# Performance work log

Measured on AMD Instinct MI355X. Metric: run time of the kernel, lower is better.

## Reference

```python
import jax, jax.numpy as jnp
import numpy as np
import math

D, H, FF = 1024, 16, 4096
B, L = 4, 1024

def setup_inputs() -> dict:
    key = jax.random.key(0)
    ks = jax.random.split(key, 20)
    g = lambda k, shp: jax.random.normal(k, shp, dtype=jnp.float32) * 0.02
    inp = {
        'x': jax.random.normal(ks[0], (B, L, D), dtype=jnp.float32),
        'encoder_output': jax.random.normal(ks[1], (B, L, D), dtype=jnp.float32),
        'src_mask': jnp.ones((1, 1, L, L), dtype=jnp.int32),
        'tgt_mask': jnp.tril(jnp.ones((L, L), dtype=jnp.int32))[None, None],
        'wq': g(ks[2], (D, D)), 'bq': jnp.zeros((D,), jnp.float32),
        'wk': g(ks[3], (D, D)), 'bk': jnp.zeros((D,), jnp.float32),
        'wv': g(ks[4], (D, D)), 'bv': jnp.zeros((D,), jnp.float32),
        'wo': g(ks[5], (D, D)), 'bo': jnp.zeros((D,), jnp.float32),
        'w1': g(ks[6], (FF, D)), 'b1': jnp.zeros((FF,), jnp.float32),
        'w2': g(ks[7], (D, FF)), 'b2': jnp.zeros((D,), jnp.float32),
        'g1': jnp.ones((D,), jnp.float32), 'be1': jnp.zeros((D,), jnp.float32),
        'g2': jnp.ones((D,), jnp.float32), 'be2': jnp.zeros((D,), jnp.float32),
    }
    return inp

def _layernorm(x, g, b, eps=1e-5):
    mu = jnp.mean(x, axis=-1, keepdims=True)
    var = jnp.var(x, axis=-1, keepdims=True)
    return (x - mu) * jax.lax.rsqrt(var + eps) * g + b

def _mha(q, k, v, mask, wq, bq, wk, bk, wv, bv, wo, bo):
    Bq, Lq, C = q.shape
    dh = C // H
    qh = (q @ wq.T + bq).reshape(Bq, Lq, H, dh)      # b q h d
    kh = (k @ wk.T + bk).reshape(Bq, -1, H, dh)       # b k h d
    vh = (v @ wv.T + bv).reshape(Bq, -1, H, dh)
    # NOTE: source scales by sqrt(C) (full model dim), not sqrt(head_dim)
    scores = jnp.einsum('bqhd,bkhd->bhqk', qh, kh) / math.sqrt(C)
    if mask is not None:
        scores = jnp.where(mask == 0, jnp.float32(-1e9), scores)
    attn = jax.nn.softmax(scores, axis=-1)
    out = jnp.einsum('bhqk,bkhd->bqhd', attn, vh).reshape(Bq, Lq, C)
    return out @ wo.T + bo

def reference(x, encoder_output, src_mask, tgt_mask,
              wq, bq, wk, bk, wv, bv, wo, bo,
              w1, b1, w2, b2, g1, be1, g2, be2):
    # self-attention (dropout identity in eval mode)
    y1 = _mha(x, x, x, tgt_mask, wq, bq, wk, bk, wv, bv, wo, bo)
    y1 = _layernorm(y1 + x, g1, be1)
    # cross-attention: source reuses attn1 weights and layer_norm1 (faithful)
    y2 = _mha(y1, encoder_output, encoder_output, src_mask, wq, bq, wk, bk, wv, bv, wo, bo)
    y2 = _layernorm(y1 + y2, g1, be1)
    # FFN + layer_norm2
    y = jax.nn.relu(y2 @ w1.T + b1) @ w2.T + b2
    return _layernorm(y2 + y, g2, be2)
```

## Files before the change

### kernel.cpp

```cpp
#include <hip/hip_runtime.h>
#include <hip/hip_bf16.h>

typedef __attribute__((ext_vector_type(8))) short short8;
typedef __attribute__((ext_vector_type(4))) float f32x4;
typedef __attribute__((ext_vector_type(4))) unsigned short ushort4v;

#define MFMA_BF16(a, b, c) __builtin_amdgcn_mfma_f32_16x16x32_bf16((a), (b), (c), 0, 0, 0)
#define AS1 __attribute__((address_space(1)))
#define AS3 __attribute__((address_space(3)))

__device__ __forceinline__ unsigned short f2b(float f) {
  unsigned u = __float_as_uint(f);
  u += 0x7fffu + ((u >> 16) & 1u);
  return (unsigned short)(u >> 16);
}

__device__ __forceinline__ size_t kpack_idx(int row, int col) {
  int b = row >> 10, l = row & 1023, h = col >> 6, d = col & 63;
  return ((size_t)(b * 16 + h) << 16) + l * 64 + (d ^ ((l & 7) << 3));
}

__global__ __launch_bounds__(256) void cast8(
    const float* s0, const float* s1, const float* s2, const float* s3,
    const float* s4, const float* s5, const float* s6, const float* s7,
    unsigned short* d0, unsigned short* d1, unsigned short* d2, unsigned short* d3,
    unsigned short* d4, unsigned short* d5, unsigned short* d6, unsigned short* d7,
    int n0, int n1, int n2, int n3, int n4, int n5, int n6, int n7) {
  const float* s; unsigned short* d; int n;
  switch (blockIdx.y) {
    case 0: s = s0; d = d0; n = n0; break;
    case 1: s = s1; d = d1; n = n1; break;
    case 2: s = s2; d = d2; n = n2; break;
    case 3: s = s3; d = d3; n = n3; break;
    case 4: s = s4; d = d4; n = n4; break;
    case 5: s = s5; d = d5; n = n5; break;
    case 6: s = s6; d = d6; n = n6; break;
    default: s = s7; d = d7; n = n7; break;
  }
  int stride = gridDim.x * blockDim.x;
  for (int i = blockIdx.x * blockDim.x + threadIdx.x; i < n; i += stride) {
    float4 v = reinterpret_cast<const float4*>(s)[i];
    ushort4v o;
    o.x = f2b(v.x); o.y = f2b(v.y); o.z = f2b(v.z); o.w = f2b(v.w);
    reinterpret_cast<ushort4v*>(d)[i] = o;
  }
}

template <int RELU, int RES, int OUTF, int OUTB, int TM>
__global__ __launch_bounds__(256) void gemm_bt(
    const unsigned short* __restrict__ A, const unsigned short* __restrict__ W,
    const float* __restrict__ bias, const float* __restrict__ resid,
    float* __restrict__ outF, unsigned short* __restrict__ outB,
    int M, int N, int K) {
  constexpr int MI = TM / 32;
  __shared__ unsigned short lA[TM * 64];
  __shared__ unsigned short lB[128 * 64];
  int nbn = N >> 7;
  int nwg = gridDim.x;
  int id = blockIdx.x;
  { int q = nwg >> 3; id = (id & 7) * q + (id >> 3); }
  int m0 = (id / nbn) * TM, n0 = (id % nbn) << 7;
  int lane = threadIdx.x & 63, wave = threadIdx.x >> 6;
  int wr = (wave >> 1) * (TM / 2), wc = (wave & 1) * 64;
  int rq = lane & 15, kq = (lane >> 4) * 8;
  int xr8 = (rq & 7) << 3;
  f32x4 acc[MI][4] = {};

  int t8 = threadIdx.x * 8;
  for (int kt = 0; kt < K; kt += 64) {
#pragma unroll
    for (int i = 0; i < MI; ++i) {
      int e = t8 + i * 2048;
      int row = e >> 6;
      int gcol = (((e >> 3) & 7) ^ (row & 7)) << 3;
      __builtin_amdgcn_global_load_lds(
          (const AS1 void*)(A + (size_t)(m0 + row) * K + kt + gcol),
          (AS3 void*)(lA + e), 16, 0, 0);
    }
#pragma unroll
    for (int i = 0; i < 4; ++i) {
      int e = t8 + i * 2048;
      int row = e >> 6;
      int gcol = (((e >> 3) & 7) ^ (row & 7)) << 3;
      __builtin_amdgcn_global_load_lds(
          (const AS1 void*)(W + (size_t)(n0 + row) * K + kt + gcol),
          (AS3 void*)(lB + e), 16, 0, 0);
    }
    __syncthreads();
#pragma unroll
    for (int s = 0; s < 2; ++s) {
      short8 af[MI], bf[4];
#pragma unroll
      for (int i = 0; i < MI; ++i)
        af[i] = *reinterpret_cast<const short8*>(lA + (wr + i * 16 + rq) * 64 + ((s * 32 + kq) ^ xr8));
#pragma unroll
      for (int j = 0; j < 4; ++j)
        bf[j] = *reinterpret_cast<const short8*>(lB + (wc + j * 16 + rq) * 64 + ((s * 32 + kq) ^ xr8));
#pragma unroll
      for (int i = 0; i < MI; ++i)
#pragma unroll
        for (int j = 0; j < 4; ++j)
          acc[i][j] = MFMA_BF16(af[i], bf[j], acc[i][j]);
    }
    __syncthreads();
  }

  int r0 = (lane >> 4) * 4;
#pragma unroll
  for (int i = 0; i < MI; ++i) {
#pragma unroll
    for (int j = 0; j < 4; ++j) {
      int row = m0 + wr + i * 16 + r0;
      int col = n0 + wc + j * 16 + rq;
      float bv = bias[col];
#pragma unroll
      for (int r = 0; r < 4; ++r) {
        float v = acc[i][j][r] + bv;
        if (RES) v += resid[(size_t)(row + r) * N + col];
        if (RELU) v = fmaxf(v, 0.0f);
        if (OUTF) outF[(size_t)(row + r) * N + col] = v;
        if (OUTB) outB[(size_t)(row + r) * N + col] = f2b(v);
      }
    }
  }
}

__global__ __launch_bounds__(256) void gemm_qkv(
    const unsigned short* __restrict__ xb, const unsigned short* __restrict__ encb,
    const unsigned short* __restrict__ wq, const unsigned short* __restrict__ wk,
    const unsigned short* __restrict__ wv,
    const float* __restrict__ bq, const float* __restrict__ bk, const float* __restrict__ bv,
    unsigned short* __restrict__ qb, unsigned short* __restrict__ kp1,
    unsigned short* __restrict__ vp1, unsigned short* __restrict__ kp2,
    unsigned short* __restrict__ vp2) {
  __shared__ unsigned short lA[128 * 64];
  __shared__ unsigned short lB[128 * 64];
  int id = blockIdx.x;
  id = (id & 7) * 160 + (id >> 3);
  int im = id / 40, jn = id % 40;
  int sel = jn >> 3;
  int m0 = im << 7, col0 = (jn & 7) << 7;
  const unsigned short* A = (sel < 3) ? xb : encb;
  const unsigned short* Wm = (sel == 0) ? wq : ((sel == 1 || sel == 3) ? wk : wv);
  const float* bias = (sel == 0) ? bq : ((sel == 1 || sel == 3) ? bk : bv);
  int lane = threadIdx.x & 63, wave = threadIdx.x >> 6;
  int wr = (wave >> 1) * 64, wc = (wave & 1) * 64;
  int rq = lane & 15, kq = (lane >> 4) * 8;
  int xr8 = (rq & 7) << 3;
  f32x4 acc[4][4] = {};

  int t8 = threadIdx.x * 8;
  for (int kt = 0; kt < 1024; kt += 64) {
#pragma unroll
    for (int i = 0; i < 4; ++i) {
      int e = t8 + i * 2048;
      int row = e >> 6;
      int gcol = (((e >> 3) & 7) ^ (row & 7)) << 3;
      __builtin_amdgcn_global_load_lds(
          (const AS1 void*)(A + (size_t)(m0 + row) * 1024 + kt + gcol),
          (AS3 void*)(lA + e), 16, 0, 0);
      __builtin_amdgcn_global_load_lds(
          (const AS1 void*)(Wm + (size_t)(col0 + row) * 1024 + kt + gcol),
          (AS3 void*)(lB + e), 16, 0, 0);
    }
    __syncthreads();
#pragma unroll
    for (int s = 0; s < 2; ++s) {
      short8 af[4], bf[4];
#pragma unroll
      for (int i = 0; i < 4; ++i)
        af[i] = *reinterpret_cast<const short8*>(lA + (wr + i * 16 + rq) * 64 + ((s * 32 + kq) ^ xr8));
#pragma unroll
      for (int j = 0; j < 4; ++j)
        bf[j] = *reinterpret_cast<const short8*>(lB + (wc + j * 16 + rq) * 64 + ((s * 32 + kq) ^ xr8));
#pragma unroll
      for (int i = 0; i < 4; ++i)
#pragma unroll
        for (int j = 0; j < 4; ++j)
          acc[i][j] = MFMA_BF16(af[i], bf[j], acc[i][j]);
    }
    __syncthreads();
  }

  unsigned short* outp = (sel == 0) ? qb : (sel == 1) ? kp1 : (sel == 2) ? vp1
                         : (sel == 3) ? kp2 : vp2;
  int pack = (sel == 0) ? 0 : ((sel == 1 || sel == 3) ? 1 : 2);
  int r0 = (lane >> 4) * 4;
#pragma unroll
  for (int i = 0; i < 4; ++i) {
#pragma unroll
    for (int j = 0; j < 4; ++j) {
      int row0 = m0 + wr + i * 16 + r0;
      int col = col0 + wc + j * 16 + rq;
      float bv = bias[col];
      if (pack == 2) {
        int b = row0 >> 10, k0 = row0 & 1023, h = col >> 6, d = col & 63;
        size_t idx = ((size_t)((b * 16 + h) * 16 + (k0 >> 6)) << 12) + d * 64 + ((k0 & 63) ^ ((d & 7) << 3));
        ushort4v o;
        o.x = f2b(acc[i][j][0] + bv);
        o.y = f2b(acc[i][j][1] + bv);
        o.z = f2b(acc[i][j][2] + bv);
        o.w = f2b(acc[i][j][3] + bv);
        *reinterpret_cast<ushort4v*>(&outp[idx]) = o;
      } else {
#pragma unroll
        for (int r = 0; r < 4; ++r) {
          int row = row0 + r;
          float v = acc[i][j][r] + bv;
          if (pack == 0) outp[(size_t)row * 1024 + col] = f2b(v);
          else outp[kpack_idx(row, col)] = f2b(v);
        }
      }
    }
  }
}

__device__ __forceinline__ void attn_step(
    const unsigned short* __restrict__ kcur, const unsigned short* __restrict__ vcur,
    unsigned short* __restrict__ plw, const short8* qf,
    f32x4* accd, float& m2, float& lsum,
    int rq, int hi, int kq, int xr, int wave, bool domask) {
  const float SC = 0.04508422f;
  f32x4 st[4];
#pragma unroll
  for (int sub = 0; sub < 4; ++sub) {
    f32x4 z = {0.f, 0.f, 0.f, 0.f};
#pragma unroll
    for (int c = 0; c < 2; ++c) {
      short8 kf = *reinterpret_cast<const short8*>(
          &kcur[(sub * 16 + rq) * 64 + ((c * 32 + hi * 8) ^ xr)]);
      z = MFMA_BF16(kf, qf[c], z);
    }
    st[sub] = z * SC;
  }
  if (domask) {
#pragma unroll
    for (int sub = 0; sub < 4; ++sub)
#pragma unroll
      for (int r = 0; r < 4; ++r)
        if (sub * 16 + hi * 4 + r > wave * 16 + rq) st[sub][r] = -1e9f;
  }
  f32x4 t0 = {fmaxf(st[0][0], st[1][0]), fmaxf(st[0][1], st[1][1]),
              fmaxf(st[0][2], st[1][2]), fmaxf(st[0][3], st[1][3])};
  f32x4 t1 = {fmaxf(st[2][0], st[3][0]), fmaxf(st[2][1], st[3][1]),
              fmaxf(st[2][2], st[3][2]), fmaxf(st[2][3], st[3][3])};
  float mx = fmaxf(fmaxf(fmaxf(t0[0], t1[0]), fmaxf(t0[1], t1[1])),
                   fmaxf(fmaxf(t0[2], t1[2]), fmaxf(t0[3], t1[3])));
  mx = fmaxf(mx, __shfl_xor(mx, 16, 64));
  mx = fmaxf(mx, __shfl_xor(mx, 32, 64));
  float mn = fmaxf(m2, mx);
  float al = exp2f(m2 - mn);
  m2 = mn;
  f32x4 e[4];
#pragma unroll
  for (int sub = 0; sub < 4; ++sub)
#pragma unroll
    for (int r = 0; r < 4; ++r) e[sub][r] = exp2f(st[sub][r] - mn);
  f32x4 s01 = e[0] + e[1], s23 = e[2] + e[3];
  f32x4 s = s01 + s23;
  float ps = (s[0] + s[1]) + (s[2] + s[3]);
  ps += __shfl_xor(ps, 16, 64);
  ps += __shfl_xor(ps, 32, 64);
  lsum = lsum * al + ps;
#pragma unroll
  for (int sub = 0; sub < 4; ++sub) {
    unsigned w0 = (unsigned)f2b(e[sub][0]) | ((unsigned)f2b(e[sub][1]) << 16);
    unsigned w1 = (unsigned)f2b(e[sub][2]) | ((unsigned)f2b(e[sub][3]) << 16);
    uint2 w = make_uint2(w0, w1);
    *reinterpret_cast<uint2*>(&plw[rq * 64 + ((sub * 16 + hi * 4) ^ xr)]) = w;
  }
  float alb[4];
#pragma unroll
  for (int r = 0; r < 4; ++r) alb[r] = __shfl(al, hi * 4 + r, 64);
#pragma unroll
  for (int d = 0; d < 4; ++d)
#pragma unroll
    for (int r = 0; r < 4; ++r) accd[d][r] *= alb[r];
  short8 pf[2];
#pragma unroll
  for (int c = 0; c < 2; ++c)
    pf[c] = *reinterpret_cast<const short8*>(&plw[rq * 64 + ((c * 32 + hi * 8) ^ xr)]);
#pragma unroll
  for (int d = 0; d < 4; ++d) {
#pragma unroll
    for (int c = 0; c < 2; ++c) {
      short8 vf = *reinterpret_cast<const short8*>(
          &vcur[(d * 16 + rq) * 64 + ((c * 32 + hi * 8) ^ xr)]);
      accd[d] = MFMA_BF16(pf[c], vf, accd[d]);
    }
  }
}

__global__ __launch_bounds__(256) void attn_kernel(
    const unsigned short* __restrict__ Q, const unsigned short* __restrict__ Kp,
    const unsigned short* __restrict__ Vp, unsigned short* __restrict__ O, int causal) {
  __shared__ unsigned short kls[2][4096];
  __shared__ unsigned short vls[2][4096];
  __shared__ unsigned short pls[4][1024];
  int id = blockIdx.x;
  int xcd = id & 7, j = id >> 3;
  int bh = xcd * 8 + (j & 7);
  int b = bh >> 4, h = bh & 15;
  int lane = threadIdx.x & 63, wave = threadIdx.x >> 6;
  int rq = lane & 15, hi = lane >> 4, kq = hi * 8;
  int xr = (rq & 7) << 3;
  int sb = wave * 1024 + lane * 8;
  const unsigned short* Kbh = Kp + ((size_t)bh << 16);
  const unsigned short* Vbh = Vp + ((size_t)bh << 16);
  unsigned short* plw = pls[wave];

  int p = j >> 3;
  int qtA = p;
  int qtB = causal ? (15 - p) : (p + 8);
  int lastA = causal ? qtA : 15;
  int nkt = causal ? (qtB + 1) : 16;

  int qrowA = qtA * 64 + wave * 16, qrowB = qtB * 64 + wave * 16;
  short8 qfA[2], qfB[2];
#pragma unroll
  for (int c = 0; c < 2; ++c) {
    qfA[c] = *reinterpret_cast<const short8*>(
        Q + (size_t)(b * 1024 + qrowA + rq) * 1024 + h * 64 + c * 32 + kq);
    qfB[c] = *reinterpret_cast<const short8*>(
        Q + (size_t)(b * 1024 + qrowB + rq) * 1024 + h * 64 + c * 32 + kq);
  }

  float mA = -1e30f, lsA = 0.f, mB = -1e30f, lsB = 0.f;
  f32x4 accA[4] = {}, accB[4] = {};

#pragma unroll
  for (int i = 0; i < 2; ++i) {
    __builtin_amdgcn_global_load_lds((const AS1 void*)(Kbh + sb + i * 512),
                                     (AS3 void*)(&kls[0][sb + i * 512]), 16, 0, 0);
    __builtin_amdgcn_global_load_lds((const AS1 void*)(Vbh + sb + i * 512),
                                     (AS3 void*)(&vls[0][sb + i * 512]), 16, 0, 0);
  }
  __syncthreads();

  int cur = 0;
  for (int kt = 0; kt < nkt; ++kt) {
    if (kt + 1 < nkt) {
      const unsigned short* kg = Kbh + (kt + 1) * 4096 + sb;
      const unsigned short* vg = Vbh + (kt + 1) * 4096 + sb;
#pragma unroll
      for (int i = 0; i < 2; ++i) {
        __builtin_amdgcn_global_load_lds((const AS1 void*)(kg + i * 512),
                                         (AS3 void*)(&kls[cur ^ 1][sb + i * 512]), 16, 0, 0);
        __builtin_amdgcn_global_load_lds((const AS1 void*)(vg + i * 512),
                                         (AS3 void*)(&vls[cur ^ 1][sb + i * 512]), 16, 0, 0);
      }
    }
    attn_step(kls[cur], vls[cur], plw, qfB, accB, mB, lsB, rq, hi, kq, xr, wave,
              causal && kt == qtB);
    if (kt <= lastA)
      attn_step(kls[cur], vls[cur], plw, qfA, accA, mA, lsA, rq, hi, kq, xr, wave,
                causal && kt == qtA);
    __syncthreads();
    cur ^= 1;
  }

  float lbA[4], lbB[4];
#pragma unroll
  for (int r = 0; r < 4; ++r) {
    lbA[r] = 1.0f / __shfl(lsA, hi * 4 + r, 64);
    lbB[r] = 1.0f / __shfl(lsB, hi * 4 + r, 64);
  }
#pragma unroll
  for (int d = 0; d < 4; ++d)
#pragma unroll
    for (int r = 0; r < 4; ++r) {
      O[(size_t)(b * 1024 + qrowA + hi * 4 + r) * 1024 + h * 64 + d * 16 + rq] =
          f2b(accA[d][r] * lbA[r]);
      O[(size_t)(b * 1024 + qrowB + hi * 4 + r) * 1024 + h * 64 + d * 16 + rq] =
          f2b(accB[d][r] * lbB[r]);
    }
}

template <int OUTF, int OUTB>
__global__ __launch_bounds__(256) void ln_kernel(const float* __restrict__ X,
                                                 const float* __restrict__ g,
                                                 const float* __restrict__ be,
                                                 float* __restrict__ outF,
                                                 unsigned short* __restrict__ outB) {
  __shared__ float red[2][4];
  int row = blockIdx.x;
  int t = threadIdx.x;
  const float* xr = X + (size_t)row * 1024;
  float4 v = reinterpret_cast<const float4*>(xr)[t];
  float s = v.x + v.y + v.z + v.w;
  float ss = v.x * v.x + v.y * v.y + v.z * v.z + v.w * v.w;
#pragma unroll
  for (int off = 1; off < 64; off <<= 1) {
    s += __shfl_xor(s, off, 64);
    ss += __shfl_xor(ss, off, 64);
  }
  int wave = t >> 6;
  if ((t & 63) == 0) { red[0][wave] = s; red[1][wave] = ss; }
  __syncthreads();
  s = red[0][0] + red[0][1] + red[0][2] + red[0][3];
  ss = red[1][0] + red[1][1] + red[1][2] + red[1][3];
  float mu = s * (1.f / 1024.f);
  float var = ss * (1.f / 1024.f) - mu * mu;
  float rs = rsqrtf(var + 1e-5f);
  float4 gv = reinterpret_cast<const float4*>(g)[t];
  float4 bv = reinterpret_cast<const float4*>(be)[t];
  float o0 = (v.x - mu) * rs * gv.x + bv.x;
  float o1 = (v.y - mu) * rs * gv.y + bv.y;
  float o2 = (v.z - mu) * rs * gv.z + bv.z;
  float o3 = (v.w - mu) * rs * gv.w + bv.w;
  if (OUTF) {
    float4 o = make_float4(o0, o1, o2, o3);
    reinterpret_cast<float4*>(outF + (size_t)row * 1024)[t] = o;
  }
  if (OUTB) {
    ushort4v o;
    o.x = f2b(o0); o.y = f2b(o1); o.z = f2b(o2); o.w = f2b(o3);
    reinterpret_cast<ushort4v*>(outB + (size_t)row * 1024)[t] = o;
  }
}

extern "C" void kernel_launch(void* const* d_in, const int* in_sizes, int n_in,
                              void* d_out, int out_size, void* d_ws, size_t ws_size,
                              hipStream_t stream) {
  const float* x   = (const float*)d_in[0];
  const float* enc = (const float*)d_in[1];
  const float* wq = (const float*)d_in[4];  const float* bq = (const float*)d_in[5];
  const float* wk = (const float*)d_in[6];  const float* bk = (const float*)d_in[7];
  const float* wv = (const float*)d_in[8];  const float* bv = (const float*)d_in[9];
  const float* wo = (const float*)d_in[10]; const float* bo = (const float*)d_in[11];
  const float* w1 = (const float*)d_in[12]; const float* b1 = (const float*)d_in[13];
  const float* w2 = (const float*)d_in[14]; const float* b2 = (const float*)d_in[15];
  const float* g1 = (const float*)d_in[16]; const float* be1 = (const float*)d_in[17];
  const float* g2 = (const float*)d_in[18]; const float* be2 = (const float*)d_in[19];
  float* out = (float*)d_out;

  const int M = 4096;
  char* ws = (char*)d_ws;
  size_t off = 0;
  auto alloc = [&](size_t bytes) -> char* {
    char* p = ws + off;
    off += (bytes + 255) & ~(size_t)255;
    return p;
  };
  unsigned short* xb   = (unsigned short*)alloc((size_t)M * 1024 * 2);
  unsigned short* encb = (unsigned short*)alloc((size_t)M * 1024 * 2);
  unsigned short* wqb  = (unsigned short*)alloc((size_t)1024 * 1024 * 2);
  unsigned short* wkb  = (unsigned short*)alloc((size_t)1024 * 1024 * 2);
  unsigned short* wvb  = (unsigned short*)alloc((size_t)1024 * 1024 * 2);
  unsigned short* wob  = (unsigned short*)alloc((size_t)1024 * 1024 * 2);
  unsigned short* w1b  = (unsigned short*)alloc((size_t)4096 * 1024 * 2);
  unsigned short* w2b  = (unsigned short*)alloc((size_t)4096 * 1024 * 2);
  unsigned short* qb   = (unsigned short*)alloc((size_t)M * 1024 * 2);
  unsigned short* kp1  = (unsigned short*)alloc((size_t)M * 1024 * 2);
  unsigned short* vp1  = (unsigned short*)alloc((size_t)M * 1024 * 2);
  unsigned short* kp2  = (unsigned short*)alloc((size_t)M * 1024 * 2);
  unsigned short* vp2  = (unsigned short*)alloc((size_t)M * 1024 * 2);
  unsigned short* ab   = (unsigned short*)alloc((size_t)M * 1024 * 2);
  float* s1 = (float*)alloc((size_t)M * 1024 * 4);
  float* y1 = (float*)alloc((size_t)M * 1024 * 4);
  unsigned short* hb = kp1;
  unsigned short* y1b = xb;
  unsigned short* y2b = qb;
  float* y2 = y1;

  dim3 b256(256);
  cast8<<<dim3(256, 8), b256, 0, stream>>>(
      x, enc, wq, wk, wv, wo, w1, w2,
      xb, encb, wqb, wkb, wvb, wob, w1b, w2b,
      M * 1024 / 4, M * 1024 / 4, 262144, 262144, 262144, 262144,
      4096 * 1024 / 4, 4096 * 1024 / 4);

  gemm_qkv<<<1280, b256, 0, stream>>>(xb, encb, wqb, wkb, wvb, bq, bk, bv,
                                      qb, kp1, vp1, kp2, vp2);

  attn_kernel<<<512, b256, 0, stream>>>(qb, kp1, vp1, ab, 1);
  gemm_bt<0, 1, 1, 0, 64><<<512, b256, 0, stream>>>(ab, wob, bo, x, s1, nullptr, M, 1024, 1024);
  ln_kernel<1, 1><<<4096, b256, 0, stream>>>(s1, g1, be1, y1, y1b);

  gemm_bt<0, 0, 0, 1, 64><<<512, b256, 0, stream>>>(y1b, wqb, bq, nullptr, nullptr, qb, M, 1024, 1024);
  attn_kernel<<<512, b256, 0, stream>>>(qb, kp2, vp2, ab, 0);
  gemm_bt<0, 1, 1, 0, 64><<<512, b256, 0, stream>>>(ab, wob, bo, y1, s1, nullptr, M, 1024, 1024);
  ln_kernel<1, 1><<<4096, b256, 0, stream>>>(s1, g1, be1, y2, y2b);

  gemm_bt<1, 0, 0, 1, 128><<<1024, b256, 0, stream>>>(y2b, w1b, b1, nullptr, nullptr, hb, M, 4096, 1024);
  gemm_bt<0, 1, 1, 0, 64><<<512, b256, 0, stream>>>(hb, w2b, b2, y2, s1, nullptr, M, 1024, 4096);
  ln_kernel<1, 0><<<4096, b256, 0, stream>>>(s1, g2, be2, out, nullptr);

  (void)in_sizes; (void)n_in; (void)out_size; (void)ws_size;
}
```

Measured before the change: 354.9 us.

## Double-buffer GEMM LDS tiles with BK=32 and add setprio around attention MFMAs

Both GEMM kernels now use two LDS buffers of K=32 slices, prefetching the next slice while computing the current one, with one barrier per step instead of two. The XOR swizzle on the LDS layout is dropped and launch bounds request 4 waves-per-EU occupancy. Attention MFMA sections are wrapped in s_setprio to favour matrix issue. Risks: an unswizzled 64-byte row stride may cause LDS bank conflicts, and halving K per step doubles the number of loop iterations and barriers.

```diff
diff --git a/kernel.cpp b/kernel.cpp
--- a/kernel.cpp
+++ b/kernel.cpp
@@ -47,14 +47,14 @@
 }
 
 template <int RELU, int RES, int OUTF, int OUTB, int TM>
-__global__ __launch_bounds__(256) void gemm_bt(
+__global__ __launch_bounds__(256, 4) void gemm_bt(
     const unsigned short* __restrict__ A, const unsigned short* __restrict__ W,
     const float* __restrict__ bias, const float* __restrict__ resid,
     float* __restrict__ outF, unsigned short* __restrict__ outB,
     int M, int N, int K) {
   constexpr int MI = TM / 32;
-  __shared__ unsigned short lA[TM * 64];
-  __shared__ unsigned short lB[128 * 64];
+  __shared__ unsigned short lA[2][TM * 32];
+  __shared__ unsigned short lB[2][128 * 32];
   int nbn = N >> 7;
   int nwg = gridDim.x;
   int id = blockIdx.x;
@@ -63,47 +63,48 @@
   int lane = threadIdx.x & 63, wave = threadIdx.x >> 6;
   int wr = (wave >> 1) * (TM / 2), wc = (wave & 1) * 64;
   int rq = lane & 15, kq = (lane >> 4) * 8;
-  int xr8 = (rq & 7) << 3;
   f32x4 acc[MI][4] = {};
 
-  int t8 = threadIdx.x * 8;
-  for (int kt = 0; kt < K; kt += 64) {
-#pragma unroll
-    for (int i = 0; i < MI; ++i) {
-      int e = t8 + i * 2048;
-      int row = e >> 6;
-      int gcol = (((e >> 3) & 7) ^ (row & 7)) << 3;
-      __builtin_amdgcn_global_load_lds(
-          (const AS1 void*)(A + (size_t)(m0 + row) * K + kt + gcol),
-          (AS3 void*)(lA + e), 16, 0, 0);
-    }
-#pragma unroll
-    for (int i = 0; i < 4; ++i) {
-      int e = t8 + i * 2048;
-      int row = e >> 6;
-      int gcol = (((e >> 3) & 7) ^ (row & 7)) << 3;
-      __builtin_amdgcn_global_load_lds(
-          (const AS1 void*)(W + (size_t)(n0 + row) * K + kt + gcol),
-          (AS3 void*)(lB + e), 16, 0, 0);
-    }
+  int e0 = threadIdx.x * 8;
+#define STAGE_BT(KT, BUF)                                                       \
+  {                                                                             \
+    _Pragma("unroll") for (int i = 0; i < TM / 64; ++i) {                       \
+      int e = e0 + i * 2048;                                                    \
+      int row = e >> 5, col = e & 31;                                           \
+      __builtin_amdgcn_global_load_lds(                                         \
+          (const AS1 void*)(A + (size_t)(m0 + row) * K + (KT) + col),           \
+          (AS3 void*)(&lA[BUF][e]), 16, 0, 0);                                  \
+    }                                                                           \
+    _Pragma("unroll") for (int i = 0; i < 2; ++i) {                             \
+      int e = e0 + i * 2048;                                                    \
+      int row = e >> 5, col = e & 31;                                           \
+      __builtin_amdgcn_global_load_lds(                                         \
+          (const AS1 void*)(W + (size_t)(n0 + row) * K + (KT) + col),           \
+          (AS3 void*)(&lB[BUF][e]), 16, 0, 0);                                  \
+    }                                                                           \
+  }
+
+  STAGE_BT(0, 0);
+  __syncthreads();
+  int nk = K >> 5;
+  for (int t = 0; t < nk; ++t) {
+    int cur = t & 1;
+    if (t + 1 < nk) STAGE_BT((t + 1) << 5, cur ^ 1);
+    short8 af[MI], bf[4];
+#pragma unroll
+    for (int i = 0; i < MI; ++i)
+      af[i] = *reinterpret_cast<const short8*>(&lA[cur][(wr + i * 16 + rq) * 32 + kq]);
+#pragma unroll
+    for (int j = 0; j < 4; ++j)
+      bf[j] = *reinterpret_cast<const short8*>(&lB[cur][(wc + j * 16 + rq) * 32 + kq]);
+#pragma unroll
+    for (int i = 0; i < MI; ++i)
+#pragma unroll
+      for (int j = 0; j < 4; ++j)
+        acc[i][j] = MFMA_BF16(af[i], bf[j], acc[i][j]);
     __syncthreads();
-#pragma unroll
-    for (int s = 0; s < 2; ++s) {
-      short8 af[MI], bf[4];
-#pragma unroll
-      for (int i = 0; i < MI; ++i)
-        af[i] = *reinterpret_cast<const short8*>(lA + (wr + i * 16 + rq) * 64 + ((s * 32 + kq) ^ xr8));
-#pragma unroll
-      for (int j = 0; j < 4; ++j)
-        bf[j] = *reinterpret_cast<const short8*>(lB + (wc + j * 16 + rq) * 64 + ((s * 32 + kq) ^ xr8));
-#pragma unroll
-      for (int i = 0; i < MI; ++i)
-#pragma unroll
-        for (int j = 0; j < 4; ++j)
-          acc[i][j] = MFMA_BF16(af[i], bf[j], acc[i][j]);
-    }
-    __syncthreads();
-  }
+  }
+#undef STAGE_BT
 
   int r0 = (lane >> 4) * 4;
 #pragma unroll
@@ -125,7 +126,7 @@
   }
 }
 
-__global__ __launch_bounds__(256) void gemm_qkv(
+__global__ __launch_bounds__(256, 4) void gemm_qkv(
     const unsigned short* __restrict__ xb, const unsigned short* __restrict__ encb,
     const unsigned short* __restrict__ wq, const unsigned short* __restrict__ wk,
     const unsigned short* __restrict__ wv,
@@ -133,8 +134,8 @@
     unsigned short* __restrict__ qb, unsigned short* __restrict__ kp1,
     unsigned short* __restrict__ vp1, unsigned short* __restrict__ kp2,
     unsigned short* __restrict__ vp2) {
-  __shared__ unsigned short lA[128 * 64];
-  __shared__ unsigned short lB[128 * 64];
+  __shared__ unsigned short lA[2][128 * 32];
+  __shared__ unsigned short lB[2][128 * 32];
   int id = blockIdx.x;
   id = (id & 7) * 160 + (id >> 3);
   int im = id / 40, jn = id % 40;
@@ -146,41 +147,43 @@
   int lane = threadIdx.x & 63, wave = threadIdx.x >> 6;
   int wr = (wave >> 1) * 64, wc = (wave & 1) * 64;
   int rq = lane & 15, kq = (lane >> 4) * 8;
-  int xr8 = (rq & 7) << 3;
   f32x4 acc[4][4] = {};
 
-  int t8 = threadIdx.x * 8;
-  for (int kt = 0; kt < 1024; kt += 64) {
-#pragma unroll
-    for (int i = 0; i < 4; ++i) {
-      int e = t8 + i * 2048;
-      int row = e >> 6;
-      int gcol = (((e >> 3) & 7) ^ (row & 7)) << 3;
-      __builtin_amdgcn_global_load_lds(
-          (const AS1 void*)(A + (size_t)(m0 + row) * 1024 + kt + gcol),
-          (AS3 void*)(lA + e), 16, 0, 0);
-      __builtin_amdgcn_global_load_lds(
-          (const AS1 void*)(Wm + (size_t)(col0 + row) * 1024 + kt + gcol),
-          (AS3 void*)(lB + e), 16, 0, 0);
-    }
+  int e0 = threadIdx.x * 8;
+#define STAGE_QKV(KT, BUF)                                                      \
+  {                                                                             \
+    _Pragma("unroll") for (int i = 0; i < 2; ++i) {                             \
+      int e = e0 + i * 2048;                                                    \
+      int row = e >> 5, col = e & 31;                                           \
+      __builtin_amdgcn_global_load_lds(                                         \
+          (const AS1 void*)(A + (size_t)(m0 + row) * 1024 + (KT) + col),        \
+          (AS3 void*)(&lA[BUF][e]), 16, 0, 0);                                  \
+      __builtin_amdgcn_global_load_lds(                                         \
+          (const AS1 void*)(Wm + (size_t)(col0 + row) * 1024 + (KT) + col),     \
+          (AS3 void*)(&lB[BUF][e]), 16, 0, 0);                                  \
+    }                                                                           \
+  }
+
+  STAGE_QKV(0, 0);
+  __syncthreads();
+  for (int t = 0; t < 32; ++t) {
+    int cur = t & 1;
+    if (t + 1 < 32) STAGE_QKV((t + 1) << 5, cur ^ 1);
+    short8 af[4], bf[4];
+#pragma unroll
+    for (int i = 0; i < 4; ++i)
+      af[i] = *reinterpret_cast<const short8*>(&lA[cur][(wr + i * 16 + rq) * 32 + kq]);
+#pragma unroll
+    for (int j = 0; j < 4; ++j)
+      bf[j] = *reinterpret_cast<const short8*>(&lB[cur][(wc + j * 16 + rq) * 32 + kq]);
+#pragma unroll
+    for (int i = 0; i < 4; ++i)
+#pragma unroll
+      for (int j = 0; j < 4; ++j)
+        acc[i][j] = MFMA_BF16(af[i], bf[j], acc[i][j]);
     __syncthreads();
-#pragma unroll
-    for (int s = 0; s < 2; ++s) {
-      short8 af[4], bf[4];
-#pragma unroll
-      for (int i = 0; i < 4; ++i)
-        af[i] = *reinterpret_cast<const short8*>(lA + (wr + i * 16 + rq) * 64 + ((s * 32 + kq) ^ xr8));
-#pragma unroll
-      for (int j = 0; j < 4; ++j)
-        bf[j] = *reinterpret_cast<const short8*>(lB + (wc + j * 16 + rq) * 64 + ((s * 32 + kq) ^ xr8));
-#pragma unroll
-      for (int i = 0; i < 4; ++i)
-#pragma unroll
-        for (int j = 0; j < 4; ++j)
-          acc[i][j] = MFMA_BF16(af[i], bf[j], acc[i][j]);
-    }
-    __syncthreads();
-  }
+  }
+#undef STAGE_QKV
 
   unsigned short* outp = (sel == 0) ? qb : (sel == 1) ? kp1 : (sel == 2) ? vp1
                          : (sel == 3) ? kp2 : vp2;
@@ -222,6 +225,7 @@
     int rq, int hi, int kq, int xr, int wave, bool domask) {
   const float SC = 0.04508422f;
   f32x4 st[4];
+  __builtin_amdgcn_s_setprio(1);
 #pragma unroll
   for (int sub = 0; sub < 4; ++sub) {
     f32x4 z = {0.f, 0.f, 0.f, 0.f};
@@ -233,6 +237,7 @@
     }
     st[sub] = z * SC;
   }
+  __builtin_amdgcn_s_setprio(0);
   if (domask) {
 #pragma unroll
     for (int sub = 0; sub < 4; ++sub)
@@ -280,6 +285,7 @@
 #pragma unroll
   for (int c = 0; c < 2; ++c)
     pf[c] = *reinterpret_cast<const short8*>(&plw[rq * 64 + ((c * 32 + hi * 8) ^ xr)]);
+  __builtin_amdgcn_s_setprio(1);
 #pragma unroll
   for (int d = 0; d < 4; ++d) {
 #pragma unroll
@@ -289,6 +295,7 @@
       accd[d] = MFMA_BF16(pf[c], vf, accd[d]);
     }
   }
+  __builtin_amdgcn_s_setprio(0);
 }
 
 __global__ __launch_bounds__(256) void attn_kernel(
```

Result: slower. 362.3 us (+2.1%).

## Double-buffer QKV GEMM LDS tiles and raise wave priority around attention MFMAs

Applied to the files above, without the earlier changes.

The QKV projection GEMM now uses two 32-wide K stages in LDS, prefetching the next tile while computing the current one, and needs one barrier per iteration instead of two. It also drops the XOR swizzle and adds a launch-bounds occupancy hint of 4. The attention step wraps its QK and PV MFMA blocks in s_setprio so those waves get issue priority. Risks: removing the swizzle may bring back LDS bank conflicts, and the smaller K step doubles the loop count.

```diff
diff --git a/kernel.cpp b/kernel.cpp
--- a/kernel.cpp
+++ b/kernel.cpp
@@ -125,7 +125,7 @@
   }
 }
 
-__global__ __launch_bounds__(256) void gemm_qkv(
+__global__ __launch_bounds__(256, 4) void gemm_qkv(
     const unsigned short* __restrict__ xb, const unsigned short* __restrict__ encb,
     const unsigned short* __restrict__ wq, const unsigned short* __restrict__ wk,
     const unsigned short* __restrict__ wv,
@@ -133,8 +133,8 @@
     unsigned short* __restrict__ qb, unsigned short* __restrict__ kp1,
     unsigned short* __restrict__ vp1, unsigned short* __restrict__ kp2,
     unsigned short* __restrict__ vp2) {
-  __shared__ unsigned short lA[128 * 64];
-  __shared__ unsigned short lB[128 * 64];
+  __shared__ unsigned short lA[2][128 * 32];
+  __shared__ unsigned short lB[2][128 * 32];
   int id = blockIdx.x;
   id = (id & 7) * 160 + (id >> 3);
   int im = id / 40, jn = id % 40;
@@ -146,41 +146,43 @@
   int lane = threadIdx.x & 63, wave = threadIdx.x >> 6;
   int wr = (wave >> 1) * 64, wc = (wave & 1) * 64;
   int rq = lane & 15, kq = (lane >> 4) * 8;
-  int xr8 = (rq & 7) << 3;
   f32x4 acc[4][4] = {};
 
-  int t8 = threadIdx.x * 8;
-  for (int kt = 0; kt < 1024; kt += 64) {
-#pragma unroll
-    for (int i = 0; i < 4; ++i) {
-      int e = t8 + i * 2048;
-      int row = e >> 6;
-      int gcol = (((e >> 3) & 7) ^ (row & 7)) << 3;
-      __builtin_amdgcn_global_load_lds(
-          (const AS1 void*)(A + (size_t)(m0 + row) * 1024 + kt + gcol),
-          (AS3 void*)(lA + e), 16, 0, 0);
-      __builtin_amdgcn_global_load_lds(
-          (const AS1 void*)(Wm + (size_t)(col0 + row) * 1024 + kt + gcol),
-          (AS3 void*)(lB + e), 16, 0, 0);
-    }
+  int e0 = threadIdx.x * 8;
+#define STAGE_QKV(KT, BUF)                                                      \
+  {                                                                             \
+    _Pragma("unroll") for (int i = 0; i < 2; ++i) {                             \
+      int e = e0 + i * 2048;                                                    \
+      int row = e >> 5, col = e & 31;                                           \
+      __builtin_amdgcn_global_load_lds(                                         \
+          (const AS1 void*)(A + (size_t)(m0 + row) * 1024 + (KT) + col),        \
+          (AS3 void*)(&lA[BUF][e]), 16, 0, 0);                                  \
+      __builtin_amdgcn_global_load_lds(                                         \
+          (const AS1 void*)(Wm + (size_t)(col0 + row) * 1024 + (KT) + col),     \
+          (AS3 void*)(&lB[BUF][e]), 16, 0, 0);                                  \
+    }                                                                           \
+  }
+
+  STAGE_QKV(0, 0);
+  __syncthreads();
+  for (int t = 0; t < 32; ++t) {
+    int cur = t & 1;
+    if (t + 1 < 32) STAGE_QKV((t + 1) << 5, cur ^ 1);
+    short8 af[4], bf[4];
+#pragma unroll
+    for (int i = 0; i < 4; ++i)
+      af[i] = *reinterpret_cast<const short8*>(&lA[cur][(wr + i * 16 + rq) * 32 + kq]);
+#pragma unroll
+    for (int j = 0; j < 4; ++j)
+      bf[j] = *reinterpret_cast<const short8*>(&lB[cur][(wc + j * 16 + rq) * 32 + kq]);
+#pragma unroll
+    for (int i = 0; i < 4; ++i)
+#pragma unroll
+      for (int j = 0; j < 4; ++j)
+        acc[i][j] = MFMA_BF16(af[i], bf[j], acc[i][j]);
     __syncthreads();
-#pragma unroll
-    for (int s = 0; s < 2; ++s) {
-      short8 af[4], bf[4];
-#pragma unroll
-      for (int i = 0; i < 4; ++i)
-        af[i] = *reinterpret_cast<const short8*>(lA + (wr + i * 16 + rq) * 64 + ((s * 32 + kq) ^ xr8));
-#pragma unroll
-      for (int j = 0; j < 4; ++j)
-        bf[j] = *reinterpret_cast<const short8*>(lB + (wc + j * 16 + rq) * 64 + ((s * 32 + kq) ^ xr8));
-#pragma unroll
-      for (int i = 0; i < 4; ++i)
-#pragma unroll
-        for (int j = 0; j < 4; ++j)
-          acc[i][j] = MFMA_BF16(af[i], bf[j], acc[i][j]);
-    }
-    __syncthreads();
-  }
+  }
+#undef STAGE_QKV
 
   unsigned short* outp = (sel == 0) ? qb : (sel == 1) ? kp1 : (sel == 2) ? vp1
                          : (sel == 3) ? kp2 : vp2;
@@ -222,6 +224,7 @@
     int rq, int hi, int kq, int xr, int wave, bool domask) {
   const float SC = 0.04508422f;
   f32x4 st[4];
+  __builtin_amdgcn_s_setprio(1);
 #pragma unroll
   for (int sub = 0; sub < 4; ++sub) {
     f32x4 z = {0.f, 0.f, 0.f, 0.f};
@@ -233,6 +236,7 @@
     }
     st[sub] = z * SC;
   }
+  __builtin_amdgcn_s_setprio(0);
   if (domask) {
 #pragma unroll
     for (int sub = 0; sub < 4; ++sub)
@@ -280,6 +284,7 @@
 #pragma unroll
   for (int c = 0; c < 2; ++c)
     pf[c] = *reinterpret_cast<const short8*>(&plw[rq * 64 + ((c * 32 + hi * 8) ^ xr)]);
+  __builtin_amdgcn_s_setprio(1);
 #pragma unroll
   for (int d = 0; d < 4; ++d) {
 #pragma unroll
@@ -289,6 +294,7 @@
       accd[d] = MFMA_BF16(pf[c], vf, accd[d]);
     }
   }
+  __builtin_amdgcn_s_setprio(0);
 }
 
 __global__ __launch_bounds__(256) void attn_kernel(
```

Result: no change. 350.5 us (-1.2%).
